# Kernel optimization log

Measured on AMD Instinct MI355X. Metric: run time of the kernel, lower is better.

The kernel has to match this reference:

```python
import jax, jax.numpy as jnp
import numpy as np

W0, W1 = 14, 14            # window size
NUM_HEADS = 12
DIM = 768
HEAD_DIM = DIM // NUM_HEADS
N_TOK = W0 * W1 + 1        # 197 (with cls token)
BATCH = 64


def _mask_1d_rel_pos_index(s):
    i = np.arange(s)
    return i[None, :] - i[:, None] + s - 1


def _add_cls(index, num_tokens, offset):
    index = index.reshape(num_tokens, num_tokens)
    new = np.zeros((num_tokens + 1, num_tokens + 1), dtype=np.int32)
    new[1:, 1:] = index
    new[0, :] = offset
    new[:, 0] = offset + 1
    new[0, 0] = offset + 2
    return new


def _build_rel_indices():
    nt = W0 * W1
    h = _mask_1d_rel_pos_index(W0).reshape(W0, 1, W0, 1)
    h = np.broadcast_to(h, (W0, W1, W0, W1))
    h_index = _add_cls(h, nt, 2 * W0 - 1)
    w = _mask_1d_rel_pos_index(W1).reshape(1, W1, 1, W1)
    w = np.broadcast_to(w, (W0, W1, W0, W1))
    w_index = _add_cls(w, nt, 2 * W1 - 1)
    return jnp.asarray(h_index), jnp.asarray(w_index)


def setup_inputs() -> dict:
    key = jax.random.key(0)
    ks = jax.random.split(key, 6)
    h_index, w_index = _build_rel_indices()
    return {
        "x": jax.random.normal(ks[0], (BATCH, N_TOK, DIM), dtype=jnp.float32),
        "qkv_w": jax.random.normal(ks[1], (3 * DIM, DIM), dtype=jnp.float32) * 0.02,
        "q_bias": jnp.zeros((DIM,), dtype=jnp.float32),
        "v_bias": jnp.zeros((DIM,), dtype=jnp.float32),
        "proj_w": jax.random.normal(ks[2], (DIM, DIM), dtype=jnp.float32) * 0.02,
        "proj_b": jnp.zeros((DIM,), dtype=jnp.float32),
        "rpb_high": jax.random.normal(ks[3], (2 * W0 + 2, NUM_HEADS), dtype=jnp.float32) * 0.02,
        "rpb_width": jax.random.normal(ks[4], (2 * W1 + 2, NUM_HEADS), dtype=jnp.float32) * 0.02,
        "h_index": h_index,
        "w_index": w_index,
    }


def reference(x, qkv_w, q_bias, v_bias, proj_w, proj_b, rpb_high, rpb_width,
              h_index, w_index):
    B, N, C = x.shape
    scale = HEAD_DIM ** (-0.5)
    # fused qkv with (q_bias, 0, v_bias) bias as in torch source
    bias = jnp.concatenate([q_bias, jnp.zeros_like(v_bias), v_bias])
    qkv = x @ qkv_w.T + bias                             # [B, N, 3*C]
    qkv = qkv.reshape(B, N, 3, NUM_HEADS, HEAD_DIM).transpose(2, 0, 3, 1, 4)
    q, k, v = qkv[0], qkv[1], qkv[2]                     # [B, H, N, hd]
    q = q * scale
    # qk_float=True -> scores in float32
    attn = jnp.einsum('bhnd,bhmd->bhnm',
                      q.astype(jnp.float32), k.astype(jnp.float32))
    # decoupled relative position bias: two embedding lookups, summed
    rpb = rpb_high[h_index] + rpb_width[w_index]         # [N, N, H]
    rpb = rpb.transpose(2, 0, 1)                         # [H, N, N]
    attn = attn + rpb[None].astype(attn.dtype)
    attn = jax.nn.softmax(attn, axis=-1).astype(x.dtype)
    out = jnp.einsum('bhnm,bhmd->bnhd', attn, v).reshape(B, N, C)
    return out @ proj_w.T + proj_b
```

## Files before the change

### kernel.cpp

```cpp
#include <hip/hip_runtime.h>
#include <hip/hip_bf16.h>
#include <cstdint>
#include <cstddef>

using fx4  = __attribute__((ext_vector_type(4))) float;
using bfx8 = __attribute__((ext_vector_type(8))) short;
using sx4  = __attribute__((ext_vector_type(4))) short;

#define DEV __device__ __forceinline__

static constexpr int BATCH = 64;
static constexpr int NTOK  = 197;
static constexpr int NH    = 12;
static constexpr int HD    = 64;
static constexpr int MROWS = BATCH * NTOK;
static constexpr int MPAD  = 12800;
static constexpr int KDIM  = 768;

DEV unsigned short f2bf(float f) {
  unsigned u = __builtin_bit_cast(unsigned, f);
  u += 0x7FFFu + ((u >> 16) & 1u);
  return (unsigned short)(u >> 16);
}

DEV void gload16(const unsigned short* g, unsigned short* l) {
  __builtin_amdgcn_global_load_lds(
      (const __attribute__((address_space(1))) unsigned int*)g,
      (__attribute__((address_space(3))) unsigned int*)l, 16, 0, 0);
}

DEV int xcd_swizzle(int orig, int nwg) {
  int q = nwg >> 3, r = nwg & 7;
  int xcd = orig & 7, lid = orig >> 3;
  return (xcd < r ? xcd * (q + 1) : r * (q + 1) + (xcd - r) * q) + lid;
}

DEV void cvt_seg(const float* __restrict__ in, unsigned short* __restrict__ out,
                 int nvec, int nvec_pad, int bseg, int nblk, int t)
{
  for (int v = bseg * 256 + t; v < nvec_pad; v += nblk * 256) {
    fx4 x = (v < nvec) ? ((const fx4*)in)[v] : fx4{0.f, 0.f, 0.f, 0.f};
    sx4 h4;
    #pragma unroll
    for (int q = 0; q < 4; q++) h4[q] = (short)f2bf(x[q]);
    ((sx4*)out)[v] = h4;
  }
}

__global__ __launch_bounds__(256)
void prologue_kernel(const float* __restrict__ x, unsigned short* __restrict__ Axb,
                     const float* __restrict__ qkvw, unsigned short* __restrict__ Bqb,
                     const float* __restrict__ projw, unsigned short* __restrict__ Bpb,
                     const float* __restrict__ rh, const float* __restrict__ rw,
                     const int* __restrict__ hidx, const int* __restrict__ widx,
                     float* __restrict__ rpb, unsigned short* __restrict__ ofb)
{
  const int blk = blockIdx.x, t = threadIdx.x;
  if (blk < 2048) {
    cvt_seg(x, Axb, MROWS * KDIM / 4, MPAD * KDIM / 4, blk, 2048, t);
  } else if (blk < 2560) {
    cvt_seg(qkvw, Bqb, 2304 * KDIM / 4, 2304 * KDIM / 4, blk - 2048, 512, t);
  } else if (blk < 2688) {
    cvt_seg(projw, Bpb, 768 * KDIM / 4, 768 * KDIM / 4, blk - 2560, 128, t);
  } else if (blk < 3200) {
    const int NN = NTOK * NTOK;
    for (int e = (blk - 2688) * 256 + t; e < NH * NN; e += 512 * 256) {
      int h = e / NN, ij = e % NN;
      rpb[e] = rh[hidx[ij] * NH + h] + rw[widx[ij] * NH + h];
    }
  } else {
    sx4* pad = (sx4*)(ofb + (size_t)MROWS * KDIM);
    const int nv = (MPAD - MROWS) * KDIM / 4;
    for (int v = (blk - 3200) * 256 + t; v < nv; v += 16 * 256)
      pad[v] = sx4{0, 0, 0, 0};
  }
}

template<int NT, int MODE>
__global__ __launch_bounds__(512, 4)
void gemm_bf16_kernel(const unsigned short* __restrict__ A,
                      const unsigned short* __restrict__ B,
                      const float* __restrict__ bias0, const float* __restrict__ bias1,
                      unsigned short* __restrict__ qb, unsigned short* __restrict__ kb,
                      unsigned short* __restrict__ vb, float* __restrict__ outp)
{
  __shared__ unsigned short At[256 * 64];
  __shared__ unsigned short Bt[128 * 64];

  const int t  = threadIdx.x;
  const int w  = t >> 6, l = t & 63;
  const int wr = w >> 1, wc = w & 1;
  const int fr = l & 15, g = l >> 4;
  const int bid = xcd_swizzle(blockIdx.x, gridDim.x);
  const int bm = bid / NT, bn = bid % NT;

  const int srow = w * 8 + (l >> 3);
  const int sgr8 = ((l & 7) ^ ((l >> 3) & 7)) * 8;

  auto STAGE = [&](int k0) {
    #pragma unroll
    for (int rd = 0; rd < 4; rd++) {
      int arow = bm * 256 + rd * 64 + srow;
      gload16(A + (size_t)arow * KDIM + k0 + sgr8, &At[(rd * 512 + w * 64) * 8]);
    }
    #pragma unroll
    for (int rd = 0; rd < 2; rd++) {
      int brow = bn * 128 + rd * 64 + srow;
      gload16(B + (size_t)brow * KDIM + k0 + sgr8, &Bt[(rd * 512 + w * 64) * 8]);
    }
  };

  fx4 acc[4][4];
  #pragma unroll
  for (int i = 0; i < 4; i++)
    #pragma unroll
    for (int j = 0; j < 4; j++) acc[i][j] = fx4{0.f, 0.f, 0.f, 0.f};

  const int a_r0 = wr * 64 + fr;
  const int b_r0 = wc * 64 + fr;
  const int swz7 = fr & 7;

  #pragma unroll 1
  for (int kt = 0; kt < 12; kt++) {
    __syncthreads();
    STAGE(kt * 64);
    __syncthreads();

    #pragma unroll
    for (int ks = 0; ks < 2; ks++) {
      const int gsw = ((ks * 4 + g) ^ swz7) * 8;
      bfx8 fb[4];
      #pragma unroll
      for (int j = 0; j < 4; j++)
        fb[j] = *(const bfx8*)&Bt[(b_r0 + j * 16) * 64 + gsw];
      #pragma unroll
      for (int i = 0; i < 4; i++) {
        bfx8 fa = *(const bfx8*)&At[(a_r0 + i * 16) * 64 + gsw];
        #pragma unroll
        for (int j = 0; j < 4; j++)
          acc[i][j] = __builtin_amdgcn_mfma_f32_16x16x32_bf16(fa, fb[j], acc[i][j], 0, 0, 0);
      }
    }
  }

  #pragma unroll
  for (int i = 0; i < 4; i++) {
    #pragma unroll
    for (int j = 0; j < 4; j++) {
      #pragma unroll
      for (int r = 0; r < 4; r++) {
        int row = bm * 256 + wr * 64 + i * 16 + g * 4 + r;
        int col = bn * 128 + wc * 64 + j * 16 + fr;
        if (row >= MROWS) continue;
        float v = acc[i][j][r];
        if (MODE == 0) {
          int which = col / 768;
          int hh = (col >> 6) % 12;
          int d  = col & 63;
          int b  = row / NTOK, n = row % NTOK;
          size_t o = (((size_t)(b * NH + hh)) * NTOK + n) * HD + d;
          if (which == 0)      qb[o] = f2bf((v + bias0[col]) * 0.125f);
          else if (which == 1) kb[o] = f2bf(v);
          else                 vb[o] = f2bf(v + bias1[col - 1536]);
        } else {
          outp[(size_t)row * 768 + col] = v + bias0[col];
        }
      }
    }
  }
}

__global__ __launch_bounds__(256)
void attn_mfma_kernel(const unsigned short* __restrict__ qf,
                      const unsigned short* __restrict__ kf,
                      const unsigned short* __restrict__ vf,
                      const float* __restrict__ rpb,
                      unsigned short* __restrict__ of)
{
  __shared__ union {
    short Kb[224 * 72];
    struct { short Pb[64 * 232]; short Vt[32 * 232]; } p;
  } u;

  const int t  = threadIdx.x;
  const int w  = t >> 6, l = t & 63;
  const int fr = l & 15, g = l >> 4;
  const int bx = xcd_swizzle(blockIdx.x, BATCH * NH * 4);
  const int b  = bx / (NH * 4);
  const int h  = (bx / 4) % NH;
  const int qt = bx & 3;
  const size_t base = ((size_t)(b * NH + h)) * NTOK * HD;
  const unsigned short* qg = qf + base;
  const unsigned short* kg = kf + base;
  const unsigned short* vg = vf + base;
  const float* rhb = rpb + (size_t)h * (NTOK * NTOK);

  const bfx8 z8 = bfx8{0,0,0,0,0,0,0,0};
  const int qrow0 = qt * 64 + w * 16 + g * 4;

  fx4 sc[14];
  #pragma unroll
  for (int j = 0; j < 14; j++) {
    int key = j * 16 + fr;
    #pragma unroll
    for (int r = 0; r < 4; r++) {
      int qrow = qrow0 + r;
      sc[j][r] = (key < NTOK && qrow < NTOK) ? rhb[qrow * NTOK + key] : 0.f;
    }
  }

  const int qrow_f = qt * 64 + w * 16 + fr;
  bfx8 aq0 = z8, aq1 = z8;
  if (qrow_f < NTOK) {
    aq0 = *(const bfx8*)(qg + (size_t)qrow_f * HD + g * 8);
    aq1 = *(const bfx8*)(qg + (size_t)qrow_f * HD + 32 + g * 8);
  }

  sx4 vreg[7];
  auto VLOAD = [&](int hf) {
    #pragma unroll
    for (int rep = 0; rep < 7; rep++) {
      int task = rep * 256 + t;
      int m  = task >> 3;
      int dq = task & 7;
      vreg[rep] = (m < NTOK)
          ? *(const sx4*)(vg + (size_t)m * HD + hf * 32 + dq * 4)
          : sx4{0, 0, 0, 0};
    }
  };
  auto VWRITE = [&]() {
    #pragma unroll
    for (int rep = 0; rep < 7; rep++) {
      int task = rep * 256 + t;
      int m  = task >> 3;
      int dq = task & 7;
      #pragma unroll
      for (int q2 = 0; q2 < 4; q2++)
        u.p.Vt[(dq * 4 + q2) * 232 + m] = vreg[rep][q2];
    }
  };

  VLOAD(0);

  {
    const int rr = t >> 3, c8 = (t & 7) * 8;
    #pragma unroll
    for (int p = 0; p < 7; p++) {
      int r = p * 32 + rr;
      bfx8 o8 = (r < NTOK) ? *(const bfx8*)(kg + (size_t)r * HD + c8) : z8;
      *(bfx8*)&u.Kb[r * 72 + c8] = o8;
    }
  }
  __syncthreads();

  __builtin_amdgcn_s_setprio(1);
  #pragma unroll
  for (int j = 0; j < 14; j++) {
    bfx8 k0 = *(const bfx8*)&u.Kb[(j * 16 + fr) * 72 + g * 8];
    bfx8 k1 = *(const bfx8*)&u.Kb[(j * 16 + fr) * 72 + 32 + g * 8];
    sc[j] = __builtin_amdgcn_mfma_f32_16x16x32_bf16(aq0, k0, sc[j], 0, 0, 0);
    sc[j] = __builtin_amdgcn_mfma_f32_16x16x32_bf16(aq1, k1, sc[j], 0, 0, 0);
  }
  __builtin_amdgcn_s_setprio(0);

  #pragma unroll
  for (int j = 12; j < 14; j++) {
    int key = j * 16 + fr;
    if (key >= NTOK) {
      #pragma unroll
      for (int r = 0; r < 4; r++) sc[j][r] = -1e30f;
    }
  }

  float inv4[4];
  #pragma unroll
  for (int r = 0; r < 4; r++) {
    float m = sc[0][r];
    #pragma unroll
    for (int j = 1; j < 14; j++) m = fmaxf(m, sc[j][r]);
    #pragma unroll
    for (int off = 1; off < 16; off <<= 1) m = fmaxf(m, __shfl_xor(m, off));
    float sum = 0.f;
    #pragma unroll
    for (int j = 0; j < 14; j++) {
      float e = __expf(sc[j][r] - m);
      sc[j][r] = e; sum += e;
    }
    #pragma unroll
    for (int off = 1; off < 16; off <<= 1) sum += __shfl_xor(sum, off);
    inv4[r] = 1.0f / sum;
  }

  __syncthreads();

  #pragma unroll
  for (int j = 0; j < 14; j++) {
    int key = j * 16 + fr;
    #pragma unroll
    for (int r = 0; r < 4; r++)
      u.p.Pb[(w * 16 + g * 4 + r) * 232 + key] = (short)f2bf(sc[j][r]);
  }
  VWRITE();
  __syncthreads();

  fx4 o2[4];
  #pragma unroll
  for (int j = 0; j < 4; j++) o2[j] = fx4{0.f, 0.f, 0.f, 0.f};

  VLOAD(1);

  __builtin_amdgcn_s_setprio(1);
  #pragma unroll
  for (int kc = 0; kc < 7; kc++) {
    bfx8 pa = *(const bfx8*)&u.p.Pb[(w * 16 + fr) * 232 + kc * 32 + g * 8];
    #pragma unroll
    for (int jj = 0; jj < 2; jj++) {
      bfx8 vbb = *(const bfx8*)&u.p.Vt[(jj * 16 + fr) * 232 + kc * 32 + g * 8];
      o2[jj] = __builtin_amdgcn_mfma_f32_16x16x32_bf16(pa, vbb, o2[jj], 0, 0, 0);
    }
  }
  __builtin_amdgcn_s_setprio(0);

  __syncthreads();
  VWRITE();
  __syncthreads();

  __builtin_amdgcn_s_setprio(1);
  #pragma unroll
  for (int kc = 0; kc < 7; kc++) {
    bfx8 pa = *(const bfx8*)&u.p.Pb[(w * 16 + fr) * 232 + kc * 32 + g * 8];
    #pragma unroll
    for (int jj = 0; jj < 2; jj++) {
      bfx8 vbb = *(const bfx8*)&u.p.Vt[(jj * 16 + fr) * 232 + kc * 32 + g * 8];
      o2[2 + jj] = __builtin_amdgcn_mfma_f32_16x16x32_bf16(pa, vbb, o2[2 + jj], 0, 0, 0);
    }
  }
  __builtin_amdgcn_s_setprio(0);

  #pragma unroll
  for (int r = 0; r < 4; r++) {
    int qrow = qt * 64 + w * 16 + g * 4 + r;
    if (qrow < NTOK) {
      float inv = inv4[r];
      #pragma unroll
      for (int j = 0; j < 4; j++)
        of[((size_t)(b * NTOK + qrow)) * 768 + h * 64 + j * 16 + fr]
            = f2bf(o2[j][r] * inv);
    }
  }
}

extern "C" void kernel_launch(void* const* d_in, const int* in_sizes, int n_in,
                              void* d_out, int out_size, void* d_ws, size_t ws_size,
                              hipStream_t stream)
{
  const float* x      = (const float*)d_in[0];
  const float* qkv_w  = (const float*)d_in[1];
  const float* q_bias = (const float*)d_in[2];
  const float* v_bias = (const float*)d_in[3];
  const float* proj_w = (const float*)d_in[4];
  const float* proj_b = (const float*)d_in[5];
  const float* rpb_h  = (const float*)d_in[6];
  const float* rpb_w  = (const float*)d_in[7];
  const int*   h_idx  = (const int*)d_in[8];
  const int*   w_idx  = (const int*)d_in[9];
  float* out = (float*)d_out;

  char* ws = (char*)d_ws;
  size_t off = 0;
  auto alloc = [&](size_t bytes) { size_t o = off; off += (bytes + 255) & ~(size_t)255; return o; };

  const size_t QKV_ELEMS = (size_t)BATCH * NH * NTOK * HD;
  unsigned short* Axb = (unsigned short*)(ws + alloc((size_t)MPAD * KDIM * 2));
  unsigned short* Bqb = (unsigned short*)(ws + alloc((size_t)2304 * KDIM * 2));
  unsigned short* Bpb = (unsigned short*)(ws + alloc((size_t)768 * KDIM * 2));
  unsigned short* qb  = (unsigned short*)(ws + alloc(QKV_ELEMS * 2));
  unsigned short* kb  = (unsigned short*)(ws + alloc(QKV_ELEMS * 2));
  unsigned short* vb  = (unsigned short*)(ws + alloc(QKV_ELEMS * 2));
  float*          rpb = (float*)(ws + alloc((size_t)NH * NTOK * NTOK * 4));
  unsigned short* ofb = (unsigned short*)(ws + alloc((size_t)MPAD * KDIM * 2));
  (void)ws_size; (void)in_sizes; (void)n_in; (void)out_size;

  prologue_kernel<<<3216, 256, 0, stream>>>(
      x, Axb, qkv_w, Bqb, proj_w, Bpb, rpb_h, rpb_w, h_idx, w_idx, rpb, ofb);
  gemm_bf16_kernel<18, 0><<<50 * 18, 512, 0, stream>>>(
      Axb, Bqb, q_bias, v_bias, qb, kb, vb, nullptr);
  attn_mfma_kernel<<<BATCH * NH * 4, 256, 0, stream>>>(qb, kb, vb, rpb, ofb);
  gemm_bf16_kernel<6, 1><<<50 * 6, 512, 0, stream>>>(
      ofb, Bpb, proj_b, nullptr, nullptr, nullptr, nullptr, out);
}
```

Measured before the change: 170.5 us.

## Double-buffer GEMM LDS tiles with K=32 steps and async prefetch

The GEMM main loop now keeps two LDS buffers with a K-step of 32 instead of one buffer with a K-step of 64. The next-but-one tile is loaded while the current one feeds the MFMAs, with explicit vmcnt waits and barriers in place of the double __syncthreads per iteration. This is meant to hide global-to-LDS load latency behind the matrix math. In exchange there are twice as many iterations, a new swizzle pattern, and the hand-written waitcnt counts must exactly match the number of outstanding loads.

```diff
diff --git a/kernel.cpp b/kernel.cpp
--- a/kernel.cpp
+++ b/kernel.cpp
@@ -84,8 +84,8 @@
                       unsigned short* __restrict__ qb, unsigned short* __restrict__ kb,
                       unsigned short* __restrict__ vb, float* __restrict__ outp)
 {
-  __shared__ unsigned short At[256 * 64];
-  __shared__ unsigned short Bt[128 * 64];
+  __shared__ unsigned short At[2][256 * 32];
+  __shared__ unsigned short Bt[2][128 * 32];
 
   const int t  = threadIdx.x;
   const int w  = t >> 6, l = t & 63;
@@ -94,20 +94,18 @@
   const int bid = xcd_swizzle(blockIdx.x, gridDim.x);
   const int bm = bid / NT, bn = bid % NT;
 
-  const int srow = w * 8 + (l >> 3);
-  const int sgr8 = ((l & 7) ^ ((l >> 3) & 7)) * 8;
-
-  auto STAGE = [&](int k0) {
-    #pragma unroll
-    for (int rd = 0; rd < 4; rd++) {
-      int arow = bm * 256 + rd * 64 + srow;
-      gload16(A + (size_t)arow * KDIM + k0 + sgr8, &At[(rd * 512 + w * 64) * 8]);
-    }
+  const int srow = w * 16 + (l >> 2);
+  const int sgr8 = ((l & 3) ^ ((l >> 3) & 3)) * 8;
+
+  auto STAGE = [&](int kt, int c) {
+    const int k0 = kt * 32;
     #pragma unroll
     for (int rd = 0; rd < 2; rd++) {
-      int brow = bn * 128 + rd * 64 + srow;
-      gload16(B + (size_t)brow * KDIM + k0 + sgr8, &Bt[(rd * 512 + w * 64) * 8]);
-    }
+      int arow = bm * 256 + rd * 128 + srow;
+      gload16(A + (size_t)arow * KDIM + k0 + sgr8, &At[c][(rd * 512 + w * 64) * 8]);
+    }
+    int brow = bn * 128 + srow;
+    gload16(B + (size_t)brow * KDIM + k0 + sgr8, &Bt[c][(w * 64) * 8]);
   };
 
   fx4 acc[4][4];
@@ -118,29 +116,36 @@
 
   const int a_r0 = wr * 64 + fr;
   const int b_r0 = wc * 64 + fr;
-  const int swz7 = fr & 7;
+  const int gsw  = (g ^ ((fr >> 1) & 3)) * 8;
+
+  STAGE(0, 0);
+  STAGE(1, 1);
 
   #pragma unroll 1
-  for (int kt = 0; kt < 12; kt++) {
-    __syncthreads();
-    STAGE(kt * 64);
-    __syncthreads();
-
-    #pragma unroll
-    for (int ks = 0; ks < 2; ks++) {
-      const int gsw = ((ks * 4 + g) ^ swz7) * 8;
-      bfx8 fb[4];
+  for (int kt = 0; kt < 24; kt++) {
+    const int c = kt & 1;
+    if (kt < 23) asm volatile("s_waitcnt vmcnt(3)" ::: "memory");
+    else         asm volatile("s_waitcnt vmcnt(0)" ::: "memory");
+    __builtin_amdgcn_s_barrier();
+    asm volatile("" ::: "memory");
+
+    bfx8 fb[4];
+    #pragma unroll
+    for (int j = 0; j < 4; j++)
+      fb[j] = *(const bfx8*)&Bt[c][(b_r0 + j * 16) * 32 + gsw];
+    #pragma unroll
+    for (int i = 0; i < 4; i++) {
+      bfx8 fa = *(const bfx8*)&At[c][(a_r0 + i * 16) * 32 + gsw];
       #pragma unroll
       for (int j = 0; j < 4; j++)
-        fb[j] = *(const bfx8*)&Bt[(b_r0 + j * 16) * 64 + gsw];
-      #pragma unroll
-      for (int i = 0; i < 4; i++) {
-        bfx8 fa = *(const bfx8*)&At[(a_r0 + i * 16) * 64 + gsw];
-        #pragma unroll
-        for (int j = 0; j < 4; j++)
-          acc[i][j] = __builtin_amdgcn_mfma_f32_16x16x32_bf16(fa, fb[j], acc[i][j], 0, 0, 0);
-      }
-    }
+        acc[i][j] = __builtin_amdgcn_mfma_f32_16x16x32_bf16(fa, fb[j], acc[i][j], 0, 0, 0);
+    }
+
+    asm volatile("s_waitcnt lgkmcnt(0)" ::: "memory");
+    __builtin_amdgcn_sched_barrier(0);
+    __builtin_amdgcn_s_barrier();
+    asm volatile("" ::: "memory");
+    if (kt + 2 < 24) STAGE(kt + 2, c);
   }
 
   #pragma unroll
```

Measured after the change: 181.0 us. 6.1% more time.
